# Kernel tuning notes

Hardware: AMD Instinct MI355X
Metric: run time of the kernel (lower is better)

The kernel has to match this reference:

```python
import jax, jax.numpy as jnp
import numpy as np

N, R = 100000, 200          # num_entities, num_relations
INIT, GC1, D = 100, 150, 200  # init_emb_size, gc1_emb_size, embedding_dim
C, K, B, NA, E, NC = 200, 5, 128, 8, 500000, 16
EPS = 1e-5


def _lrelu(x):
    return jnp.where(x >= 0, x, 0.01 * x)


def _bn(x, g, b):
    # eval-mode BatchNorm1d with running_mean=0, running_var=1
    return x * (g / jnp.sqrt(jnp.asarray(1.0 + EPS, x.dtype))) + b


def _gcn(x, W, bias, alpha, edge_index, edge_rel):
    # A = coo(edge_index, alpha[edge_rel]); out = (A + A^T) @ (x @ W) + bias
    alp = alpha[edge_rel, 0]              # [E]
    support = x @ W                       # [N, F]
    row, col = edge_index[0], edge_index[1]
    w = alp[:, None]
    out = jnp.zeros_like(support)
    out = out.at[row].add(w * support[col])
    out = out.at[col].add(w * support[row])
    return out + bias


def setup_inputs():
    key = jax.random.key(0)
    ks = iter(jax.random.split(key, 40))
    rn = lambda sh: 0.05 * jax.random.normal(next(ks), sh, dtype=jnp.float32)
    inp = {}
    inp["e1"] = jax.random.randint(next(ks), (B, 1), 0, N)
    inp["rel"] = jax.random.randint(next(ks), (B, 1), 0, R)
    inp["attr"] = jax.random.randint(next(ks), (B, 1, NA), 0, N)
    inp["X"] = jnp.arange(N)
    inp["edge_index"] = jax.random.randint(next(ks), (2, E), 0, N)
    inp["edge_rel"] = jax.random.randint(next(ks), (E,), 0, R)
    inp["emb_e"] = rn((N, INIT))
    inp["emb_rel"] = rn((R, D))
    inp["alpha1"] = rn((R + 1, 1))
    inp["alpha2"] = rn((R + 1, 1))
    inp["gc1_W"] = rn((INIT, GC1)); inp["gc1_b"] = rn((GC1,))
    inp["gc2_W"] = rn((GC1, D)); inp["gc2_b"] = rn((D,))
    inp["bn3_g"] = jnp.ones(GC1); inp["bn3_b"] = jnp.zeros(GC1)
    inp["bn4_g"] = jnp.ones(D); inp["bn4_b"] = jnp.zeros(D)
    inp["bn0_g"] = jnp.ones(2); inp["bn0_b"] = jnp.zeros(2)
    inp["conv_w"] = rn((C, 2, K)); inp["conv_b"] = rn((C,))
    inp["bn1_g"] = jnp.ones(C); inp["bn1_b"] = jnp.zeros(C)
    inp["fc_w"] = rn((D, C * D)); inp["fc_b"] = rn((D,))
    inp["bn2_g"] = jnp.ones(D); inp["bn2_b"] = jnp.zeros(D)
    inp["bi_w"] = rn((D, D)); inp["bi_b"] = rn((D,))
    inp["si_w"] = rn((D, D)); inp["si_b"] = rn((D,))
    inp["cs_w"] = rn((D, 2 * D)); inp["cs_b"] = rn((D,))
    inp["fc2_w"] = rn((NC, D)); inp["fc2_b"] = rn((NC,))
    return inp


def reference(e1, rel, attr, X, edge_index, edge_rel, emb_e, emb_rel, alpha1, alpha2,
              gc1_W, gc1_b, gc2_W, gc2_b, bn3_g, bn3_b, bn4_g, bn4_b, bn0_g, bn0_b,
              conv_w, conv_b, bn1_g, bn1_b, fc_w, fc_b, bn2_g, bn2_b,
              bi_w, bi_b, si_w, si_b, cs_w, cs_b, fc2_w, fc2_b):
    emb_initial = emb_e[X]                                  # [N, INIT]
    x = _gcn(emb_initial, gc1_W, gc1_b, alpha1, edge_index, edge_rel)
    x = jnp.tanh(_bn(x, bn3_g, bn3_b))                      # [N, GC1]
    x = _gcn(x, gc2_W, gc2_b, alpha2, edge_index, edge_rel)
    all_emb = jnp.tanh(_bn(x, bn4_g, bn4_b))                # [N, D]

    e1_emb = all_emb[e1]                                    # [B, 1, D]
    rel_emb = emb_rel[rel]                                  # [B, 1, D]
    s = jnp.concatenate([e1_emb, rel_emb], axis=1)          # [B, 2, D]
    s = _bn(s, bn0_g[None, :, None], bn0_b[None, :, None])
    x = jax.lax.conv_general_dilated(s, conv_w, (1,), [(K // 2, K // 2)],
                                     dimension_numbers=("NCH", "OIH", "NCH"))
    x = x + conv_b[None, :, None]                           # [B, C, D]
    x = jax.nn.relu(_bn(x, bn1_g[None, :, None], bn1_b[None, :, None]))
    x = x.reshape(B, C * D) @ fc_w.T + fc_b                 # [B, D]
    x = jax.nn.relu(_bn(x, bn2_g, bn2_b))                   # user_embedding

    feats = all_emb[attr][:, 0]                             # [B, NA, D]
    ssum = feats.sum(axis=1)                                # [B, D]
    deep = 0.5 * (ssum ** 2 - (feats ** 2).sum(axis=1))     # FM interaction
    nfm = _lrelu(deep @ bi_w.T + bi_b) + _lrelu(ssum @ si_w.T + si_b)
    user = _lrelu(jnp.concatenate([nfm, x], axis=-1) @ cs_w.T + cs_b)  # [B, D]

    pred = jax.nn.sigmoid(user @ all_emb.T)                 # [B, N]
    clusters = jax.nn.sigmoid(user @ fc2_w.T + fc2_b)       # [B, NC]
    return pred, clusters
```

## Files before the change

kernel.cpp:

```cpp
#include <hip/hip_runtime.h>
#include <hip/hip_bf16.h>
#include <math.h>

#define NNODES 100000
#define INIT_F 100
#define GC1_F  150
#define D_F    200
#define CCH    200
#define BB     128
#define NA_    8
#define EDG    500000
#define NCL    16

#define MROWS  100032
#define MT_    (MROWS/64)

#define KPE    104
#define KP1    128
#define KP2    160
#define KPP    224
#define FCK    40000

#define NPB    256
#define NBUK   ((NNODES + NPB - 1)/NPB)
#define BCAP   4096

#define ALO ((long)128*KPP)
#define BLO ((long)256*KPP)

typedef __attribute__((ext_vector_type(8))) __bf16 bf16x8;
typedef __attribute__((ext_vector_type(4))) float  f32x4;

__device__ __forceinline__ float fast_tanh(float z){
  float ex = __expf(2.f*z);
  return 1.f - 2.f/(ex + 1.f);
}


__global__ __launch_bounds__(256) void bucket_a_k(
    const int* __restrict__ ei, const int* __restrict__ erel,
    int* __restrict__ bcur, int2* __restrict__ blist)
{
  __shared__ int hist[NBUK];
  int t = threadIdx.x;
  for (int i = t; i < NBUK; i += 256) hist[i] = 0;
  __syncthreads();
  int e0 = blockIdx.x*1024;
  int rr[4], cc[4], pl[4], rkA[4], rkB[4];
  #pragma unroll
  for (int i = 0; i < 4; i++){
    int e = e0 + i*256 + t;
    bool ok = e < EDG;
    rr[i] = ok ? ei[e]       : -1;
    cc[i] = ok ? ei[EDG + e] : 0;
    pl[i] = (ok ? erel[e] : 0) << 17;
    if (ok){
      rkA[i] = atomicAdd(&hist[rr[i] >> 8], 1);
      rkB[i] = atomicAdd(&hist[cc[i] >> 8], 1);
    }
  }
  __syncthreads();
  for (int i = t; i < NBUK; i += 256){
    int c = hist[i];
    hist[i] = c ? atomicAdd(&bcur[i], c) : 0;
  }
  __syncthreads();
  #pragma unroll
  for (int i = 0; i < 4; i++){
    if (rr[i] < 0) continue;
    int bA = rr[i] >> 8, bB = cc[i] >> 8;
    int sA = hist[bA] + rkA[i];
    int sB = hist[bB] + rkB[i];
    if (sA < BCAP) blist[(long)bA*BCAP + sA] = make_int2(rr[i], cc[i] | pl[i]);
    if (sB < BCAP) blist[(long)bB*BCAP + sB] = make_int2(cc[i], rr[i] | pl[i]);
  }
}

__global__ __launch_bounds__(256) void bucket_b_k(
    const int2* __restrict__ blist, const int* __restrict__ bcur,
    unsigned* __restrict__ adjW, int* __restrict__ start_, int* __restrict__ deg_)
{
  __shared__ int cnt[NPB];
  __shared__ int sc[NPB];
  int b = blockIdx.x, t = threadIdx.x;
  cnt[t] = 0;
  __syncthreads();
  int n = min(bcur[b], BCAP);
  const int2* bl = blist + (long)b*BCAP;
  for (int i = t; i < n; i += 256) atomicAdd(&cnt[bl[i].x & (NPB-1)], 1);
  __syncthreads();
  int v = cnt[t]; sc[t] = v; __syncthreads();
  for (int off = 1; off < NPB; off <<= 1){
    int x = (t >= off) ? sc[t-off] : 0;
    __syncthreads();
    sc[t] += x; __syncthreads();
  }
  int excl = sc[t] - v;
  int node = b*NPB + t;
  if (node < NNODES){ start_[node] = b*BCAP + excl; deg_[node] = v; }
  cnt[t] = excl;
  __syncthreads();
  for (int i = t; i < n; i += 256){
    int2 rec = bl[i];
    int s = atomicAdd(&cnt[rec.x & (NPB-1)], 1);
    adjW[(long)b*BCAP + s] = (unsigned)rec.y;
  }
}


template<int G, int LPG, int PIN, int KP, int PHO>
__global__ __launch_bounds__(1024) void gcn_layer_k(
    const __bf16* __restrict__ X, const int* __restrict__ start,
    const int* __restrict__ degv, const unsigned* __restrict__ adjW,
    const float* __restrict__ alpha,
    const __bf16* __restrict__ Bt, __bf16* __restrict__ C,
    const float* __restrict__ gb, const float* __restrict__ bng,
    const float* __restrict__ bnb, int M, int N)
{
  constexpr int KPAD = KP + 8;
  __shared__ __bf16 As[64][KPAD];
  int w = threadIdx.x >> 6;
  int lane = threadIdx.x & 63;
  int vbase = blockIdx.x*64;
  int grp = lane / LPG;
  int li  = lane - grp*LPG;
  bool act = grp < G;

  for (int q4 = 0; q4 < 4; q4++){
    int row = w*4 + q4;
    int v = vbase + row;
    float acc[8] = {};
    if (v < NNODES){
      int s = start[v], e = s + degv[v];
      for (int jb = s; jb < e; jb += 4*G){
        int u[4]; float wt[4];
        #pragma unroll
        for (int q = 0; q < 4; q++){
          int j = jb + grp + q*G;
          u[q] = 0; wt[q] = 0.f;
          if (act && j < e){ unsigned pr = adjW[j]; u[q] = pr & 0x1FFFF; wt[q] = alpha[pr >> 17]; }
        }
        bf16x8 rows[4];
        #pragma unroll
        for (int q = 0; q < 4; q++)
          rows[q] = *(const bf16x8*)(X + (long)u[q]*PIN + li*8);
        #pragma unroll
        for (int q = 0; q < 4; q++)
          #pragma unroll
          for (int i = 0; i < 8; i++)
            acc[i] += wt[q]*(float)rows[q][i];
      }
      #pragma unroll
      for (int g = 1; g < G; g++)
        #pragma unroll
        for (int i = 0; i < 8; i++)
          acc[i] += __shfl(acc[i], lane + g*LPG, 64);
    }
    if (lane < LPG){
      bf16x8 o;
      #pragma unroll
      for (int i = 0; i < 8; i++) o[i] = (__bf16)acc[i];
      *(bf16x8*)(&As[row][lane*8]) = o;
    } else if (lane < KP/8){
      bf16x8 o = {};
      *(bf16x8*)(&As[row][lane*8]) = o;
    }
  }
  __syncthreads();

  int wrow = w & 3, wcol = w >> 2;
  int n0 = wcol*64;
  if (n0 >= PHO) return;
  int ml = lane & 15, kq = lane >> 4;
  int m0 = wrow*16;
  const __bf16* Bp = Bt + (long)(n0 + ml)*KP + kq*8;
  f32x4 acc2[4] = {};
  #pragma unroll
  for (int k0 = 0; k0 < KP; k0 += 32){
    bf16x8 a = *(const bf16x8*)(&As[m0 + ml][kq*8 + k0]);
    #pragma unroll
    for (int t = 0; t < 4; t++){
      bf16x8 b = *(const bf16x8*)(Bp + (long)t*16*KP + k0);
      acc2[t] = __builtin_amdgcn_mfma_f32_16x16x32_bf16(a, b, acc2[t], 0, 0, 0);
    }
  }
  const float inv = rsqrtf(1.0f + 1e-5f);
  int mr = vbase + m0 + kq*4;
  #pragma unroll
  for (int t = 0; t < 4; t++){
    int gn = n0 + t*16 + ml;
    if (gn >= PHO) continue;
    bool real = gn < N;
    float gbb = real ? gb[gn] : 0.f;
    float sc  = real ? bng[gn]*inv : 0.f;
    float bb_ = real ? bnb[gn] : 0.f;
    #pragma unroll
    for (int r = 0; r < 4; r++){
      int gm = mr + r;
      if (gm < M){
        float xg = real ? fast_tanh((acc2[t][r] + gbb)*sc + bb_) : 0.f;
        C[(long)gm*PHO + gn] = (__bf16)xg;
      }
    }
  }
}


template<int KP, int ACT, int WPB>
__global__ __launch_bounds__(WPB*64) void mfma_gemm(
    const __bf16* __restrict__ A, const __bf16* __restrict__ Bt,
    float* __restrict__ C, long ldc, int M, int N)
{
  int w = threadIdx.x >> 6, l = threadIdx.x & 63;
  int m0 = blockIdx.y*(WPB*16) + w*16;
  int n0 = blockIdx.x*64;
  int ml = l & 15, kq = l >> 4;
  const __bf16* Ap = A  + (long)(m0 + ml)*KP + kq*8;
  const __bf16* Bp = Bt + (long)(n0 + ml)*KP + kq*8;
  f32x4 acc[4] = {};
  #pragma unroll
  for (int k0 = 0; k0 < KP; k0 += 32){
    bf16x8 a = *(const bf16x8*)(Ap + k0);
    #pragma unroll
    for (int t = 0; t < 4; t++){
      bf16x8 b = *(const bf16x8*)(Bp + (long)t*16*KP + k0);
      acc[t] = __builtin_amdgcn_mfma_f32_16x16x32_bf16(a, b, acc[t], 0, 0, 0);
    }
  }
  int mr = m0 + kq*4;
  #pragma unroll
  for (int t = 0; t < 4; t++){
    int gn = n0 + t*16 + ml;
    if (gn >= N) continue;
    #pragma unroll
    for (int r = 0; r < 4; r++){
      int gm = mr + r;
      if (gm < M){
        float x = acc[t][r];
        if (ACT == 2) x = 1.f/(1.f + __expf(-x));
        C[(long)gm*ldc + gn] = x;
      }
    }
  }
}


__global__ __launch_bounds__(256) void mfma_fc_k(
    const __bf16* __restrict__ A, const __bf16* __restrict__ Bt,
    float* __restrict__ C, int M, int N, int klen)
{
  int w = threadIdx.x >> 6, l = threadIdx.x & 63;
  int m0 = blockIdx.y*64 + w*16;
  int n0 = blockIdx.x*128;
  long kb = (long)blockIdx.z * klen;
  int ml = l & 15, kq = l >> 4;
  const __bf16* Ap = A  + (long)(m0 + ml)*FCK + kb + kq*8;
  const __bf16* Bp = Bt + (long)(n0 + ml)*FCK + kb + kq*8;
  f32x4 acc[2][4] = {};
  #pragma unroll 2
  for (int k0 = 0; k0 < klen; k0 += 32){
    bf16x8 a = *(const bf16x8*)(Ap + k0);
    #pragma unroll
    for (int c = 0; c < 2; c++)
      #pragma unroll
      for (int t = 0; t < 4; t++){
        bf16x8 b = *(const bf16x8*)(Bp + (long)(c*64 + t*16)*FCK + k0);
        acc[c][t] = __builtin_amdgcn_mfma_f32_16x16x32_bf16(a, b, acc[c][t], 0, 0, 0);
      }
  }
  int mr = m0 + kq*4;
  #pragma unroll
  for (int c = 0; c < 2; c++)
    #pragma unroll
    for (int t = 0; t < 4; t++){
      int gn = n0 + c*64 + t*16 + ml;
      if (gn >= N) continue;
      #pragma unroll
      for (int r = 0; r < 4; r++){
        int gm = mr + r;
        if (gm < M) atomicAdd(&C[(long)gm*N + gn], acc[c][t][r]);
      }
    }
}


template<int NPROD, int COMBINE, bool SPLITOUT>
__global__ __launch_bounds__(256) void mfma_head_k(
    const __bf16* __restrict__ A0, const __bf16* __restrict__ B0,
    const __bf16* __restrict__ A1, const __bf16* __restrict__ B1,
    const float* __restrict__ bias0, const float* __restrict__ bias1,
    float* __restrict__ outF, __bf16* __restrict__ outS,
    int ldc, int N)
{
  int w = threadIdx.x >> 6, l = threadIdx.x & 63;
  int m0 = blockIdx.y*64 + w*16;
  int n0 = blockIdx.x*64;
  int ml = l & 15, kq = l >> 4;
  long aoff = (long)(m0 + ml)*KPP + kq*8;
  long boff = (long)(n0 + ml)*KPP + kq*8;
  f32x4 accA[4] = {}, accB[4] = {};
  #pragma unroll
  for (int k0 = 0; k0 < KPP; k0 += 32){
    bf16x8 ah = *(const bf16x8*)(A0 + aoff + k0);
    bf16x8 al = *(const bf16x8*)(A0 + ALO + aoff + k0);
    #pragma unroll
    for (int t = 0; t < 4; t++){
      bf16x8 bh = *(const bf16x8*)(B0 + boff + (long)t*16*KPP + k0);
      bf16x8 bl = *(const bf16x8*)(B0 + BLO + boff + (long)t*16*KPP + k0);
      accA[t] = __builtin_amdgcn_mfma_f32_16x16x32_bf16(ah, bh, accA[t], 0, 0, 0);
      accA[t] = __builtin_amdgcn_mfma_f32_16x16x32_bf16(al, bh, accA[t], 0, 0, 0);
      accA[t] = __builtin_amdgcn_mfma_f32_16x16x32_bf16(ah, bl, accA[t], 0, 0, 0);
    }
    if constexpr (NPROD == 2){
      bf16x8 ch = *(const bf16x8*)(A1 + aoff + k0);
      bf16x8 cl = *(const bf16x8*)(A1 + ALO + aoff + k0);
      #pragma unroll
      for (int t = 0; t < 4; t++){
        bf16x8 bh = *(const bf16x8*)(B1 + boff + (long)t*16*KPP + k0);
        bf16x8 bl = *(const bf16x8*)(B1 + BLO + boff + (long)t*16*KPP + k0);
        accB[t] = __builtin_amdgcn_mfma_f32_16x16x32_bf16(ch, bh, accB[t], 0, 0, 0);
        accB[t] = __builtin_amdgcn_mfma_f32_16x16x32_bf16(cl, bh, accB[t], 0, 0, 0);
        accB[t] = __builtin_amdgcn_mfma_f32_16x16x32_bf16(ch, bl, accB[t], 0, 0, 0);
      }
    }
  }
  int mr = m0 + kq*4;
  #pragma unroll
  for (int t = 0; t < 4; t++){
    int gn = n0 + t*16 + ml;
    if (SPLITOUT){ if (gn >= KPP) continue; }
    else         { if (gn >= N)   continue; }
    bool real = gn < N;
    float bb0 = real ? bias0[gn] : 0.f;
    float bb1 = (COMBINE == 0 && real) ? bias1[gn] : 0.f;
    #pragma unroll
    for (int r = 0; r < 4; r++){
      int gm = mr + r;
      float x;
      if (COMBINE == 0){
        float xa = accA[t][r] + bb0; xa = (xa >= 0.f) ? xa : 0.01f*xa;
        float xb = accB[t][r] + bb1; xb = (xb >= 0.f) ? xb : 0.01f*xb;
        x = xa + xb;
      } else if (COMBINE == 1){
        x = accA[t][r] + accB[t][r] + bb0;
        x = (x >= 0.f) ? x : 0.01f*x;
      } else {
        x = accA[t][r] + bb0;
        x = 1.f/(1.f + __expf(-x));
      }
      if (!real) x = 0.f;
      if (SPLITOUT){
        __bf16 h = (__bf16)x;
        outS[(long)gm*KPP + gn] = h;
        outS[ALO + (long)gm*KPP + gn] = (__bf16)(x - (float)h);
      } else {
        outF[(long)gm*ldc + gn] = x;
      }
    }
  }
}


__global__ __launch_bounds__(256) void emb_to_bf16_k(const float* __restrict__ src,
                                                     __bf16* __restrict__ dst){
  int lane = threadIdx.x & 63;
  int half = lane >> 5, l = lane & 31;
  long r = (long)blockIdx.x*8 + (threadIdx.x >> 6)*2 + half;
  if (r >= NNODES || l >= 26) return;
  float4 v = make_float4(0.f, 0.f, 0.f, 0.f);
  if (l < 25) v = *(const float4*)(src + r*INIT_F + l*4);
  __bf16 o[4] __attribute__((aligned(8))) =
      {(__bf16)v.x, (__bf16)v.y, (__bf16)v.z, (__bf16)v.w};
  *reinterpret_cast<uint2*>(dst + r*KPE + l*4) = *reinterpret_cast<const uint2*>(o);
}

__global__ void transpose_w_k(const float* __restrict__ W, __bf16* __restrict__ Bt,
                              int K, int N, int Kp){
  int n = blockIdx.x;
  for (int k = threadIdx.x; k < Kp; k += blockDim.x){
    float v = (k < K && n < N) ? W[(long)k*N + n] : 0.f;
    Bt[(long)n*Kp + k] = (__bf16)v;
  }
}

__global__ void f32_to_bf16_flat_k(const float4* __restrict__ src,
                                   __bf16* __restrict__ dst, long n4){
  long i = (long)blockIdx.x*256 + threadIdx.x;
  if (i >= n4) return;
  float4 v = src[i];
  __bf16 o[4] __attribute__((aligned(8))) =
      {(__bf16)v.x, (__bf16)v.y, (__bf16)v.z, (__bf16)v.w};
  *reinterpret_cast<uint2*>(dst + i*4) = *reinterpret_cast<const uint2*>(o);
}

__global__ void head_wsplit_k(const float* __restrict__ bi, const float* __restrict__ si,
                              const float* __restrict__ cs, const float* __restrict__ fc2,
                              __bf16* __restrict__ W){
  int k = threadIdx.x; if (k >= KPP) return;
  int n = blockIdx.x;
  int mat = blockIdx.y;
  float v = 0.f;
  if (k < D_F){
    if      (mat == 0){ if (n < D_F) v = bi[(long)n*D_F + k]; }
    else if (mat == 1){ if (n < D_F) v = si[(long)n*D_F + k]; }
    else if (mat == 2){ if (n < D_F) v = cs[(long)n*2*D_F + k]; }
    else if (mat == 3){ if (n < D_F) v = cs[(long)n*2*D_F + D_F + k]; }
    else              { if (n < NCL) v = fc2[(long)n*D_F + k]; }
  }
  __bf16 h = (__bf16)v;
  long base = (long)mat*2*BLO + (long)n*KPP + k;
  W[base]       = h;
  W[base + BLO] = (__bf16)(v - (float)h);
}


__global__ void conv_bn_relu_k(const int* __restrict__ e1, const int* __restrict__ rel,
                               const __bf16* __restrict__ AEh, const float* __restrict__ embrel,
                               const float* __restrict__ g0, const float* __restrict__ b0,
                               const float* __restrict__ cw, const float* __restrict__ cb,
                               const float* __restrict__ g1, const float* __restrict__ b1,
                               __bf16* __restrict__ out){
  __shared__ float sh[2][D_F];
  int b = blockIdx.y, c0 = blockIdx.x*8, t = threadIdx.x;
  const float inv = rsqrtf(1.0f + 1e-5f);
  if (t < D_F){
    sh[0][t] = (float)AEh[(long)e1[b]*KPP + t] * (g0[0]*inv) + b0[0];
    sh[1][t] = embrel[(long)rel[b]*D_F + t]    * (g0[1]*inv) + b0[1];
  }
  __syncthreads();
  if (t >= D_F) return;
  for (int cc = 0; cc < 8; cc++){
    int c = c0 + cc;
    float sum = cb[c];
    #pragma unroll
    for (int i = 0; i < 2; i++){
      #pragma unroll
      for (int k = 0; k < 5; k++){
        int h = t + k - 2;
        float sv = (h >= 0 && h < D_F) ? sh[i][h] : 0.f;
        sum += sv * cw[(c*2+i)*5 + k];
      }
    }
    float x = sum * (g1[c]*inv) + b1[c];
    out[((long)b*CCH + c)*D_F + t] = (__bf16)fmaxf(x, 0.f);
  }
}

__global__ void fc_fin_k(const float* __restrict__ raw, const float* __restrict__ fb,
                         const float* __restrict__ g, const float* __restrict__ bb,
                         __bf16* __restrict__ x2s){
  int b = blockIdx.x, t = threadIdx.x;
  if (t >= KPP) return;
  float x = 0.f;
  if (t < D_F){
    const float inv = rsqrtf(1.0f + 1e-5f);
    x = (raw[b*D_F + t] + fb[t]) * (g[t]*inv) + bb[t];
    x = fmaxf(x, 0.f);
  }
  __bf16 h = (__bf16)x;
  x2s[(long)b*KPP + t] = h;
  x2s[ALO + (long)b*KPP + t] = (__bf16)(x - (float)h);
}

__global__ void feats_k(const int* __restrict__ attr, const __bf16* __restrict__ AEh,
                        __bf16* __restrict__ hA){
  int b = blockIdx.x, t = threadIdx.x;
  if (t >= KPP) return;
  float s = 0.f, sq = 0.f;
  if (t < D_F){
    #pragma unroll
    for (int a = 0; a < NA_; a++){
      int id = attr[b*NA_ + a];
      float v = (float)AEh[(long)id*KPP + t];
      s += v; sq += v*v;
    }
  }
  float dp = 0.5f*(s*s - sq);
  long o = (long)b*KPP + t;
  __bf16 hd = (__bf16)dp;
  hA[o]            = hd;
  hA[o + ALO]      = (__bf16)(dp - (float)hd);
  __bf16 hs = (__bf16)s;
  hA[o + 2*ALO]    = hs;
  hA[o + 3*ALO]    = (__bf16)(s - (float)hs);
}


extern "C" void kernel_launch(void* const* d_in, const int* in_sizes, int n_in,
                              void* d_out, int out_size, void* d_ws, size_t ws_size,
                              hipStream_t stream) {
  const int* e1       = (const int*)d_in[0];
  const int* rel      = (const int*)d_in[1];
  const int* attr     = (const int*)d_in[2];
  const int* ei       = (const int*)d_in[4];
  const int* erel     = (const int*)d_in[5];
  const float* emb_e  = (const float*)d_in[6];
  const float* embrel = (const float*)d_in[7];
  const float* alpha1 = (const float*)d_in[8];
  const float* alpha2 = (const float*)d_in[9];
  const float* gc1_W  = (const float*)d_in[10];
  const float* gc1_b  = (const float*)d_in[11];
  const float* gc2_W  = (const float*)d_in[12];
  const float* gc2_b  = (const float*)d_in[13];
  const float* bn3_g  = (const float*)d_in[14];
  const float* bn3_b  = (const float*)d_in[15];
  const float* bn4_g  = (const float*)d_in[16];
  const float* bn4_b  = (const float*)d_in[17];
  const float* bn0_g  = (const float*)d_in[18];
  const float* bn0_b  = (const float*)d_in[19];
  const float* conv_w = (const float*)d_in[20];
  const float* conv_b = (const float*)d_in[21];
  const float* bn1_g  = (const float*)d_in[22];
  const float* bn1_b  = (const float*)d_in[23];
  const float* fc_w   = (const float*)d_in[24];
  const float* fc_b   = (const float*)d_in[25];
  const float* bn2_g  = (const float*)d_in[26];
  const float* bn2_b  = (const float*)d_in[27];
  const float* bi_w   = (const float*)d_in[28];
  const float* bi_b   = (const float*)d_in[29];
  const float* si_w   = (const float*)d_in[30];
  const float* si_b   = (const float*)d_in[31];
  const float* cs_w   = (const float*)d_in[32];
  const float* cs_b   = (const float*)d_in[33];
  const float* fc2_w  = (const float*)d_in[34];
  const float* fc2_b  = (const float*)d_in[35];

  float* pred_out = (float*)d_out;
  float* clus_out = (float*)d_out + (long)BB*NNODES;

  char* w = (char*)d_ws;
  size_t off = 0;
  auto alloc = [&](size_t bytes) -> void* {
    off = (off + 255) & ~(size_t)255;
    void* p = w + off;
    off += bytes;
    return p;
  };
  __bf16* AEh  = (__bf16*)alloc((size_t)MROWS*KPP*2);
  void* bufA   = alloc((size_t)MROWS*KPE*2);
  void* bufB   = alloc((size_t)BB*FCK*2);
  __bf16* H1h  = (__bf16*)alloc((size_t)MROWS*KP2*2);

  int* bcur   = (int*)alloc((size_t)NBUK*4);
  int* start_ = (int*)alloc((size_t)NNODES*4);
  int* deg    = (int*)alloc((size_t)NNODES*4);
  int2* blist = (int2*)alloc((size_t)NBUK*BCAP*8);
  unsigned* adjW = (unsigned*)alloc((size_t)NBUK*BCAP*4);
  __bf16* Bt1 = (__bf16*)alloc((size_t)256*KP1*2);
  __bf16* Bt2 = (__bf16*)alloc((size_t)256*KP2*2);
  __bf16* headW = (__bf16*)alloc((size_t)5*2*256*KPP*2);
  __bf16* headA = (__bf16*)alloc((size_t)5*2*128*KPP*2);
  float* x2raw  = (float*)alloc((size_t)BB*D_F*4);

  __bf16* emb_h   = (__bf16*)bufA;
  __bf16* fcBt    = (__bf16*)bufA;
  __bf16* convout = (__bf16*)bufB;

  auto HAp = [&](int slot){ return headA + (size_t)slot*2*ALO; };
  auto HWp = [&](int mat){ return headW + (size_t)mat*2*BLO; };

  const int MT = MROWS/64;

  hipMemsetAsync(bcur, 0, (size_t)NBUK*4, stream);
  hipMemsetAsync(x2raw, 0, (size_t)BB*D_F*4, stream);
  bucket_a_k<<<(EDG + 1023)/1024, 256, 0, stream>>>(ei, erel, bcur, blist);
  bucket_b_k<<<NBUK, 256, 0, stream>>>(blist, bcur, adjW, start_, deg);

  emb_to_bf16_k<<<(NNODES + 7)/8, 256, 0, stream>>>(emb_e, emb_h);
  transpose_w_k<<<256, 128, 0, stream>>>(gc1_W, Bt1, INIT_F, GC1_F, KP1);
  transpose_w_k<<<256, 128, 0, stream>>>(gc2_W, Bt2, GC1_F, D_F, KP2);
  head_wsplit_k<<<dim3(256,5), 256, 0, stream>>>(bi_w, si_w, cs_w, fc2_w, headW);

  gcn_layer_k<4,13,KPE,KP1,KP2><<<MT, 1024, 0, stream>>>(
      emb_h, start_, deg, adjW, alpha1, Bt1, H1h, gc1_b, bn3_g, bn3_b, NNODES, GC1_F);

  gcn_layer_k<3,20,KP2,KP2,KPP><<<MT, 1024, 0, stream>>>(
      H1h, start_, deg, adjW, alpha2, Bt2, AEh, gc2_b, bn4_g, bn4_b, NNODES, D_F);

  {
    dim3 grid(CCH/8, BB);
    conv_bn_relu_k<<<grid, 256, 0, stream>>>(e1, rel, AEh, embrel, bn0_g, bn0_b,
                                             conv_w, conv_b, bn1_g, bn1_b, convout);
  }
  {
    long n4 = (long)D_F*FCK/4;
    f32_to_bf16_flat_k<<<(int)((n4 + 255)/256), 256, 0, stream>>>(
        (const float4*)fc_w, fcBt, n4);
  }
  {
    dim3 grid(2, 2, 125);
    mfma_fc_k<<<grid, 256, 0, stream>>>(convout, fcBt, x2raw, BB, D_F, 320);
  }
  fc_fin_k<<<BB, 256, 0, stream>>>(x2raw, fc_b, bn2_g, bn2_b, HAp(2));

  feats_k<<<BB, 256, 0, stream>>>(attr, AEh, headA);
  {
    dim3 grid(4, 2);
    mfma_head_k<2,0,true><<<grid, 256, 0, stream>>>(
        HAp(0), HWp(0), HAp(1), HWp(1), bi_b, si_b, nullptr, HAp(3), 0, D_F);
    mfma_head_k<2,1,true><<<grid, 256, 0, stream>>>(
        HAp(3), HWp(2), HAp(2), HWp(3), cs_b, nullptr, nullptr, HAp(4), 0, D_F);
  }

  {
    dim3 grid(MT, 1);
    mfma_gemm<KPP,2,8><<<grid, 512, 0, stream>>>(HAp(4), AEh, pred_out, NNODES, BB, NNODES);
  }
  {
    dim3 grid(1, 2);
    mfma_head_k<1,2,false><<<grid, 256, 0, stream>>>(
        HAp(4), HWp(4), nullptr, nullptr, fc2_b, nullptr, clus_out, nullptr, NCL, NCL);
  }
}
```

Before: 609.8 us.

## Shrink GCN blocks to 32 rows, prefetch adjacency, stage output through LDS

The fused GCN gather+GEMM kernel now uses 512-thread blocks covering 32 nodes with a launch-bounds occupancy hint. It loads start/degree vectors once per wave and software-prefetches the next adjacency chunk, including across node boundaries, to hide the dependent-load latency. The epilogue writes results into LDS and then stores full rows with coalesced 16-byte writes instead of scattered 2-byte stores. This relies on NNODES being divisible by 32 and drops the M bounds check, and it adds extra syncs and register pressure.

```diff
diff --git a/kernel.cpp b/kernel.cpp
--- a/kernel.cpp
+++ b/kernel.cpp
@@ -109,99 +109,133 @@
 
 
 template<int G, int LPG, int PIN, int KP, int PHO>
-__global__ __launch_bounds__(1024) void gcn_layer_k(
+__global__ __launch_bounds__(512, 6) void gcn_layer_k(
     const __bf16* __restrict__ X, const int* __restrict__ start,
     const int* __restrict__ degv, const unsigned* __restrict__ adjW,
     const float* __restrict__ alpha,
     const __bf16* __restrict__ Bt, __bf16* __restrict__ C,
     const float* __restrict__ gb, const float* __restrict__ bng,
-    const float* __restrict__ bnb, int M, int N)
+    const float* __restrict__ bnb, int N)
 {
   constexpr int KPAD = KP + 8;
-  __shared__ __bf16 As[64][KPAD];
-  int w = threadIdx.x >> 6;
-  int lane = threadIdx.x & 63;
-  int vbase = blockIdx.x*64;
+  constexpr int LSZ = (KPAD > PHO) ? KPAD : PHO;
+  __shared__ __bf16 lds[32 * LSZ];
+  int tid = threadIdx.x;
+  int w = tid >> 6;
+  int lane = tid & 63;
+  int vbase = blockIdx.x*32;
   int grp = lane / LPG;
   int li  = lane - grp*LPG;
   bool act = grp < G;
 
+  int v0 = vbase + w*4;
+  int4 sv4 = *(const int4*)(start + v0);
+  int4 dv4 = *(const int4*)(degv + v0);
+  int sA[4] = {sv4.x, sv4.y, sv4.z, sv4.w};
+  int eA[4] = {sv4.x + dv4.x, sv4.y + dv4.y, sv4.z + dv4.z, sv4.w + dv4.w};
+
+  unsigned prn[4];
+  #pragma unroll
+  for (int q = 0; q < 4; q++){
+    int j = sA[0] + grp + q*G;
+    prn[q] = (act && j < eA[0]) ? adjW[j] : 0u;
+  }
+  #pragma unroll
   for (int q4 = 0; q4 < 4; q4++){
-    int row = w*4 + q4;
-    int v = vbase + row;
+    int s = sA[q4], e = eA[q4];
+    unsigned prc[4] = {prn[0], prn[1], prn[2], prn[3]};
+    if (q4 < 3){
+      #pragma unroll
+      for (int q = 0; q < 4; q++){
+        int j = sA[q4+1] + grp + q*G;
+        prn[q] = (act && j < eA[q4+1]) ? adjW[j] : 0u;
+      }
+    }
     float acc[8] = {};
-    if (v < NNODES){
-      int s = start[v], e = s + degv[v];
-      for (int jb = s; jb < e; jb += 4*G){
-        int u[4]; float wt[4];
+    for (int jb = s; jb < e; jb += 4*G){
+      int u[4]; float wt[4];
+      #pragma unroll
+      for (int q = 0; q < 4; q++){
+        int j = jb + grp + q*G;
+        u[q]  = prc[q] & 0x1FFFF;
+        wt[q] = (act && j < e) ? alpha[prc[q] >> 17] : 0.f;
+      }
+      if (jb + 4*G < e){
         #pragma unroll
         for (int q = 0; q < 4; q++){
-          int j = jb + grp + q*G;
-          u[q] = 0; wt[q] = 0.f;
-          if (act && j < e){ unsigned pr = adjW[j]; u[q] = pr & 0x1FFFF; wt[q] = alpha[pr >> 17]; }
+          int j = jb + 4*G + grp + q*G;
+          prc[q] = (act && j < e) ? adjW[j] : 0u;
         }
-        bf16x8 rows[4];
-        #pragma unroll
-        for (int q = 0; q < 4; q++)
-          rows[q] = *(const bf16x8*)(X + (long)u[q]*PIN + li*8);
-        #pragma unroll
-        for (int q = 0; q < 4; q++)
-          #pragma unroll
-          for (int i = 0; i < 8; i++)
-            acc[i] += wt[q]*(float)rows[q][i];
-      }
-      #pragma unroll
-      for (int g = 1; g < G; g++)
+      }
+      bf16x8 rows[4];
+      #pragma unroll
+      for (int q = 0; q < 4; q++)
+        rows[q] = *(const bf16x8*)(X + (long)u[q]*PIN + li*8);
+      #pragma unroll
+      for (int q = 0; q < 4; q++)
         #pragma unroll
         for (int i = 0; i < 8; i++)
-          acc[i] += __shfl(acc[i], lane + g*LPG, 64);
-    }
+          acc[i] += wt[q]*(float)rows[q][i];
+    }
+    #pragma unroll
+    for (int g = 1; g < G; g++)
+      #pragma unroll
+      for (int i = 0; i < 8; i++)
+        acc[i] += __shfl(acc[i], lane + g*LPG, 64);
+    int row = w*4 + q4;
     if (lane < LPG){
       bf16x8 o;
       #pragma unroll
       for (int i = 0; i < 8; i++) o[i] = (__bf16)acc[i];
-      *(bf16x8*)(&As[row][lane*8]) = o;
+      *(bf16x8*)(&lds[row*KPAD + lane*8]) = o;
     } else if (lane < KP/8){
       bf16x8 o = {};
-      *(bf16x8*)(&As[row][lane*8]) = o;
-    }
-  }
-  __syncthreads();
-
-  int wrow = w & 3, wcol = w >> 2;
+      *(bf16x8*)(&lds[row*KPAD + lane*8]) = o;
+    }
+  }
+  __syncthreads();
+
+  int wrow = w & 1, wcol = w >> 1;
   int n0 = wcol*64;
-  if (n0 >= PHO) return;
   int ml = lane & 15, kq = lane >> 4;
   int m0 = wrow*16;
-  const __bf16* Bp = Bt + (long)(n0 + ml)*KP + kq*8;
   f32x4 acc2[4] = {};
-  #pragma unroll
-  for (int k0 = 0; k0 < KP; k0 += 32){
-    bf16x8 a = *(const bf16x8*)(&As[m0 + ml][kq*8 + k0]);
+  if (n0 < PHO){
+    const __bf16* Bp = Bt + (long)(n0 + ml)*KP + kq*8;
+    #pragma unroll
+    for (int k0 = 0; k0 < KP; k0 += 32){
+      bf16x8 a = *(const bf16x8*)(&lds[(m0 + ml)*KPAD + kq*8 + k0]);
+      #pragma unroll
+      for (int t = 0; t < 4; t++){
+        bf16x8 b = *(const bf16x8*)(Bp + (long)t*16*KP + k0);
+        acc2[t] = __builtin_amdgcn_mfma_f32_16x16x32_bf16(a, b, acc2[t], 0, 0, 0);
+      }
+    }
+  }
+  __syncthreads();
+  if (n0 < PHO){
+    const float inv = rsqrtf(1.0f + 1e-5f);
+    int mr = m0 + kq*4;
     #pragma unroll
     for (int t = 0; t < 4; t++){
-      bf16x8 b = *(const bf16x8*)(Bp + (long)t*16*KP + k0);
-      acc2[t] = __builtin_amdgcn_mfma_f32_16x16x32_bf16(a, b, acc2[t], 0, 0, 0);
-    }
-  }
-  const float inv = rsqrtf(1.0f + 1e-5f);
-  int mr = vbase + m0 + kq*4;
-  #pragma unroll
-  for (int t = 0; t < 4; t++){
-    int gn = n0 + t*16 + ml;
-    if (gn >= PHO) continue;
-    bool real = gn < N;
-    float gbb = real ? gb[gn] : 0.f;
-    float sc  = real ? bng[gn]*inv : 0.f;
-    float bb_ = real ? bnb[gn] : 0.f;
-    #pragma unroll
-    for (int r = 0; r < 4; r++){
-      int gm = mr + r;
-      if (gm < M){
+      int gn = n0 + t*16 + ml;
+      if (gn >= PHO) continue;
+      bool real = gn < N;
+      float gbb = real ? gb[gn] : 0.f;
+      float sc  = real ? bng[gn]*inv : 0.f;
+      float bb_ = real ? bnb[gn] : 0.f;
+      #pragma unroll
+      for (int r = 0; r < 4; r++){
         float xg = real ? fast_tanh((acc2[t][r] + gbb)*sc + bb_) : 0.f;
-        C[(long)gm*PHO + gn] = (__bf16)xg;
-      }
-    }
+        lds[(mr + r)*PHO + gn] = (__bf16)xg;
+      }
+    }
+  }
+  __syncthreads();
+  for (int c = tid; c < 32*(PHO/8); c += 512){
+    int row = c / (PHO/8), c8 = c - row*(PHO/8);
+    *(bf16x8*)(C + (long)(vbase + row)*PHO + c8*8) =
+        *(const bf16x8*)(&lds[row*PHO + c8*8]);
   }
 }
 
@@ -560,6 +594,7 @@
   auto HWp = [&](int mat){ return headW + (size_t)mat*2*BLO; };
 
   const int MT = MROWS/64;
+  const int MT32 = NNODES/32;
 
   hipMemsetAsync(bcur, 0, (size_t)NBUK*4, stream);
   hipMemsetAsync(x2raw, 0, (size_t)BB*D_F*4, stream);
@@ -571,11 +606,11 @@
   transpose_w_k<<<256, 128, 0, stream>>>(gc2_W, Bt2, GC1_F, D_F, KP2);
   head_wsplit_k<<<dim3(256,5), 256, 0, stream>>>(bi_w, si_w, cs_w, fc2_w, headW);
 
-  gcn_layer_k<4,13,KPE,KP1,KP2><<<MT, 1024, 0, stream>>>(
-      emb_h, start_, deg, adjW, alpha1, Bt1, H1h, gc1_b, bn3_g, bn3_b, NNODES, GC1_F);
-
-  gcn_layer_k<3,20,KP2,KP2,KPP><<<MT, 1024, 0, stream>>>(
-      H1h, start_, deg, adjW, alpha2, Bt2, AEh, gc2_b, bn4_g, bn4_b, NNODES, D_F);
+  gcn_layer_k<4,13,KPE,KP1,KP2><<<MT32, 512, 0, stream>>>(
+      emb_h, start_, deg, adjW, alpha1, Bt1, H1h, gc1_b, bn3_g, bn3_b, GC1_F);
+
+  gcn_layer_k<3,20,KP2,KP2,KPP><<<MT32, 512, 0, stream>>>(
+      H1h, start_, deg, adjW, alpha2, Bt2, AEh, gc2_b, bn4_g, bn4_b, D_F);
 
   {
     dim3 grid(CCH/8, BB);
```

Result: faster. 578.4 us (-5.2%).
